# Performance work log

Hardware: AMD Instinct MI355X
Metric: run time of the kernel (lower is better)

Reference implementation:

```python
import jax, jax.numpy as jnp
import numpy as np

HEIGHT = 108
WIDTH = 108
LEN_CLASSES = 7
EPS = 1e-5


def layout_bbox(pred, H, W):
    # pred: [B, O, 4 + LEN_CLASSES]
    bbox = pred[..., :4]
    cls_prob = pred[..., 4:]  # [B,O,7]
    x_c = bbox[..., 0] * W   # [B,O]
    y_c = bbox[..., 1] * H
    w = bbox[..., 2] * W
    h = bbox[..., 3] * H
    x1 = (x_c - 0.5 * w)[:, :, None, None]  # [B,O,1,1]
    x2 = (x_c + 0.5 * w)[:, :, None, None]
    y1 = (y_c - 0.5 * h)[:, :, None, None]
    y2 = (y_c + 0.5 * h)[:, :, None, None]
    xt = jnp.arange(W, dtype=pred.dtype)[None, None, None, :]  # [1,1,1,W]
    yt = jnp.arange(H, dtype=pred.dtype)[None, None, :, None]  # [1,1,H,1]
    x1d = xt - x1  # [B,O,1,W]
    x2d = x2 - xt
    y1d = yt - y1  # [B,O,H,1]
    y2d = y2 - yt
    # min(relu(d), 1) == clip(d, 0, 1)
    yband = jnp.clip(y1d, 0.0, 1.0) * jnp.clip(y2d, 0.0, 1.0)  # [B,O,H,1]
    xband = jnp.clip(x1d, 0.0, 1.0) * jnp.clip(x2d, 0.0, 1.0)  # [B,O,1,W]
    x1_line = jax.nn.relu(1.0 - jnp.abs(x1d)) * yband  # [B,O,H,W]
    x2_line = jax.nn.relu(1.0 - jnp.abs(x2d)) * yband
    y1_line = jax.nn.relu(1.0 - jnp.abs(y1d)) * xband
    y2_line = jax.nn.relu(1.0 - jnp.abs(y2d)) * xband
    xy_max = jnp.maximum(jnp.maximum(x1_line, x2_line), jnp.maximum(y1_line, y2_line))  # [B,O,H,W]
    spatial = xy_max[..., None] * cls_prob[:, :, None, None, :]  # [B,O,H,W,7]
    return jnp.max(spatial, axis=1)  # [B,H,W,7]


def bn(x, g, b, axes):
    m = jnp.mean(x, axis=axes, keepdims=True)
    v = jnp.var(x, axis=axes, keepdims=True)
    shape = [1] * x.ndim
    shape[1 if x.ndim == 4 else -1] = -1
    return (x - m) * jax.lax.rsqrt(v + EPS) * g.reshape(shape) + b.reshape(shape)


def conv2d(x, w, b, stride):
    y = jax.lax.conv_general_dilated(x, w, (stride, stride), 'VALID',
                                     dimension_numbers=('NCHW', 'OIHW', 'NCHW'))
    return y + b[None, :, None, None]


def setup_inputs() -> dict:
    key = jax.random.key(0)
    ks = jax.random.split(key, 16)
    B, O = 64, 16
    d = {}
    d['image'] = jax.random.uniform(ks[0], (B, O, 4 + LEN_CLASSES), dtype=jnp.float32)
    d['conv1_w'] = jax.random.normal(ks[1], (32, LEN_CLASSES, 5, 5), jnp.float32) * 0.05
    d['conv1_b'] = jnp.zeros((32,), jnp.float32)
    d['bn1_g'] = jnp.ones((32,), jnp.float32)
    d['bn1_b'] = jnp.zeros((32,), jnp.float32)
    d['conv2_w'] = jax.random.normal(ks[2], (64, 32, 5, 5), jnp.float32) * 0.03
    d['conv2_b'] = jnp.zeros((64,), jnp.float32)
    d['bn2_g'] = jnp.ones((64,), jnp.float32)
    d['bn2_b'] = jnp.zeros((64,), jnp.float32)
    d['fc1_w'] = jax.random.normal(ks[3], (512, 36864), jnp.float32) * 0.005
    d['fc1_b'] = jnp.zeros((512,), jnp.float32)
    d['bn3_g'] = jnp.ones((512,), jnp.float32)
    d['bn3_b'] = jnp.zeros((512,), jnp.float32)
    d['fc2_w'] = jax.random.normal(ks[4], (1, 512), jnp.float32) * 0.04
    d['fc2_b'] = jnp.zeros((1,), jnp.float32)
    return d


def reference(image, conv1_w, conv1_b, bn1_g, bn1_b, conv2_w, conv2_b, bn2_g, bn2_b,
              fc1_w, fc1_b, bn3_g, bn3_b, fc2_w, fc2_b):
    # layout_bbox(image, WIDTH, HEIGHT): output_height=WIDTH, output_width=HEIGHT (both 108)
    layout = layout_bbox(image, WIDTH, HEIGHT)           # [B,108,108,7]
    x = jnp.transpose(layout, (0, 3, 1, 2))              # [B,7,108,108]
    x = conv2d(x, conv1_w, conv1_b, 2)                   # [B,32,52,52]
    x = bn(x, bn1_g, bn1_b, (0, 2, 3))
    x = jax.nn.leaky_relu(x, 0.2)
    x = conv2d(x, conv2_w, conv2_b, 2)                   # [B,64,24,24]
    x = bn(x, bn2_g, bn2_b, (0, 2, 3))
    x = jax.nn.leaky_relu(x, 0.2)
    x = x.reshape(x.shape[0], -1)                        # [B,36864]
    x = x @ fc1_w.T + fc1_b                              # [B,512]
    x = bn(x, bn3_g, bn3_b, (0,))
    x = jax.nn.leaky_relu(x, 0.2)
    x = x @ fc2_w.T + fc2_b                              # [B,1]
    return jax.nn.sigmoid(x)
```

## Files before the change

kernel.cpp:

```cpp
#include <hip/hip_runtime.h>
#include <hip/hip_bf16.h>


typedef unsigned short u16;
typedef __attribute__((ext_vector_type(8))) short bf8_t;
typedef __attribute__((ext_vector_type(4))) float f4_t;
#define MFMA16(a, b, c) __builtin_amdgcn_mfma_f32_16x16x32_bf16(a, b, c, 0, 0, 0)

#define LEAKY(v) (fmaxf((v), 0.2f * (v)))
#define CLIP01(v) fminf(fmaxf((v), 0.0f), 1.0f)

__device__ inline unsigned f2bf(float f) {
  unsigned u = __float_as_uint(f);
  return (u + 0x7FFFu + ((u >> 16) & 1u)) >> 16;
}
__device__ inline float bf2f(unsigned u) {
  return __uint_as_float(u << 16);
}

constexpr int HW = 108;
constexpr int NOBJ = 16;
constexpr int NCLS = 7;

__global__ __launch_bounds__(128) void layout_kernel(
    const float* __restrict__ image, u16* __restrict__ lay8) {
  int h = blockIdx.x, b = blockIdx.y;
  __shared__ float sIm[NOBJ * 11];
  int tid = threadIdx.x;
  for (int i = tid; i < NOBJ * 11; i += 128) sIm[i] = image[b * NOBJ * 11 + i];
  __syncthreads();
  int w = tid;
  if (w >= HW) return;
  float best[NCLS];
#pragma unroll
  for (int c = 0; c < NCLS; ++c) best[c] = 0.0f;
  float fw = (float)w, fh = (float)h;
  for (int o = 0; o < NOBJ; ++o) {
    const float* p = &sIm[o * 11];
    float xc = p[0] * 108.0f, yc = p[1] * 108.0f;
    float wd = p[2] * 108.0f, hd = p[3] * 108.0f;
    float x1 = xc - 0.5f * wd, x2 = xc + 0.5f * wd;
    float y1 = yc - 0.5f * hd, y2 = yc + 0.5f * hd;
    float x1d = fw - x1, x2d = x2 - fw;
    float y1d = fh - y1, y2d = y2 - fh;
    float yband = CLIP01(y1d) * CLIP01(y2d);
    float xband = CLIP01(x1d) * CLIP01(x2d);
    float x1l = fmaxf(1.0f - fabsf(x1d), 0.0f) * yband;
    float x2l = fmaxf(1.0f - fabsf(x2d), 0.0f) * yband;
    float y1l = fmaxf(1.0f - fabsf(y1d), 0.0f) * xband;
    float y2l = fmaxf(1.0f - fabsf(y2d), 0.0f) * xband;
    float xy = fmaxf(fmaxf(x1l, x2l), fmaxf(y1l, y2l));
#pragma unroll
    for (int c = 0; c < NCLS; ++c) best[c] = fmaxf(best[c], xy * p[4 + c]);
  }
  unsigned p0 = f2bf(best[0]) | (f2bf(best[1]) << 16);
  unsigned p1 = f2bf(best[2]) | (f2bf(best[3]) << 16);
  unsigned p2 = f2bf(best[4]) | (f2bf(best[5]) << 16);
  unsigned p3 = f2bf(best[6]);
  uint4 st = {p0, p1, p2, p3};
  ((uint4*)lay8)[b * 11664 + h * 108 + w] = st;
}

__global__ __launch_bounds__(256) void wprep_kernel(
    const float* __restrict__ w1, const float* __restrict__ w2,
    u16* __restrict__ wB1, u16* __restrict__ wB2) {
  int i = blockIdx.x * 256 + threadIdx.x;
  if (i < 7168) {
    int co = i / 224, k = i % 224;
    int chunk = k >> 5, kk = k & 31, tl = kk >> 3, ci = kk & 7;
    int tap = chunk * 4 + tl;
    unsigned v = 0;
    if (tap < 25 && ci < 7) v = f2bf(w1[co * 175 + ci * 25 + tap]);
    wB1[i] = (u16)v;
  } else {
    int j = i - 7168;
    int tap = j / 2048, r = j % 2048, co = r >> 5, ci = r & 31;
    wB2[j] = (u16)f2bf(w2[co * 800 + ci * 25 + tap]);
  }
}

__global__ __launch_bounds__(128) void conv1_mfma(
    const u16* __restrict__ lay8, const u16* __restrict__ wB1,
    u16* __restrict__ x1r, float* __restrict__ bn1sum,
    float* __restrict__ bn1sq) {
  int strip = blockIdx.x, b = blockIdx.y;
  int tid = threadIdx.x;
  int lane = tid & 63, wv = tid >> 6;
  int f = lane & 15, q = lane >> 4;
  int co = wv * 16 + f;
  int pbase[13];
#pragma unroll
  for (int t = 0; t < 13; ++t) {
    int P = strip * 208 + t * 16 + f;
    int oh = P / 52, ow = P - oh * 52;
    pbase[t] = (oh * 2 * 108 + ow * 2) * 8;
  }
  const u16* lb = lay8 + (size_t)b * 93312;
  f4_t acc[13];
#pragma unroll
  for (int t = 0; t < 13; ++t) acc[t] = {0.f, 0.f, 0.f, 0.f};
#pragma unroll
  for (int chunk = 0; chunk < 7; ++chunk) {
    int tap = chunk * 4 + q;
    tap = tap > 24 ? 24 : tap;
    int kh = tap / 5, kw = tap - kh * 5;
    int toff = (kh * 108 + kw) * 8;
    bf8_t bf = *(const bf8_t*)&wB1[co * 224 + chunk * 32 + q * 8];
    bf8_t af[13];
#pragma unroll
    for (int t = 0; t < 13; ++t) af[t] = *(const bf8_t*)&lb[pbase[t] + toff];
#pragma unroll
    for (int t = 0; t < 13; ++t) acc[t] = MFMA16(af[t], bf, acc[t]);
  }
  u16* ob = x1r + (size_t)b * 86528;
  float s = 0.f, sq = 0.f;
#pragma unroll
  for (int t = 0; t < 13; ++t) {
#pragma unroll
    for (int r = 0; r < 4; ++r) {
      float v = acc[t][r];
      s += v;
      sq += v * v;
      int P = strip * 208 + t * 16 + q * 4 + r;
      ob[P * 32 + co] = (u16)f2bf(v);
    }
  }
  s += __shfl_xor(s, 16);
  s += __shfl_xor(s, 32);
  sq += __shfl_xor(sq, 16);
  sq += __shfl_xor(sq, 32);
  if (lane < 16) {
    atomicAdd(&bn1sum[co], s);
    atomicAdd(&bn1sq[co], sq);
  }
}

__global__ void bn_finalize_kernel(
    const float* __restrict__ sum, const float* __restrict__ sumsq,
    const float* __restrict__ g, const float* __restrict__ bb, float invN,
    int C, float* __restrict__ scale, float* __restrict__ shift) {
  int c = threadIdx.x;
  if (c < C) {
    float mean = sum[c] * invN;
    float var = sumsq[c] * invN - mean * mean;
    float sc = g[c] * rsqrtf(var + 1e-5f);
    scale[c] = sc;
    shift[c] = bb[c] - mean * sc;
  }
}

__global__ __launch_bounds__(256) void bnapply1_kernel(
    const u16* __restrict__ x1r, const float* __restrict__ sc,
    const float* __restrict__ sh, u16* __restrict__ x1b) {
  int idx = blockIdx.x * 256 + threadIdx.x;
  int base = idx * 8, c0 = base & 31;
  uint4 in = *(const uint4*)&x1r[base];
  unsigned w[4] = {in.x, in.y, in.z, in.w};
  unsigned out[4];
#pragma unroll
  for (int j = 0; j < 4; ++j) {
    float a = bf2f(w[j] & 0xffffu);
    float bq = bf2f(w[j] >> 16);
    a = LEAKY(fmaf(a, sc[c0 + 2 * j], sh[c0 + 2 * j]));
    bq = LEAKY(fmaf(bq, sc[c0 + 2 * j + 1], sh[c0 + 2 * j + 1]));
    out[j] = f2bf(a) | (f2bf(bq) << 16);
  }
  uint4 st = {out[0], out[1], out[2], out[3]};
  *(uint4*)&x1b[base] = st;
}

__global__ __launch_bounds__(256) void conv2_mfma(
    const u16* __restrict__ x1b, const u16* __restrict__ wB2,
    float* __restrict__ x2c, float* __restrict__ bn2sum,
    float* __restrict__ bn2sq) {
  int strip = blockIdx.x, b = blockIdx.y;
  int tid = threadIdx.x;
  int lane = tid & 63, wv = tid >> 6;
  int f = lane & 15, q = lane >> 4;
  int mbase = (wv >> 1) * 3, nbase = (wv & 1) * 2;
  int pbase[3];
#pragma unroll
  for (int t = 0; t < 3; ++t) {
    int P = strip * 96 + (mbase + t) * 16 + f;
    int oh = P / 24, ow = P - oh * 24;
    pbase[t] = (oh * 2 * 52 + ow * 2) * 32 + q * 8;
  }
  const u16* xb = x1b + (size_t)b * 86528;
  f4_t acc[3][2];
#pragma unroll
  for (int t = 0; t < 3; ++t)
#pragma unroll
    for (int n = 0; n < 2; ++n) acc[t][n] = {0.f, 0.f, 0.f, 0.f};
#pragma unroll
  for (int tap = 0; tap < 25; ++tap) {
    int kh = tap / 5, kw = tap - kh * 5;
    int toff = (kh * 52 + kw) * 32;
    bf8_t bfr[2];
#pragma unroll
    for (int n = 0; n < 2; ++n)
      bfr[n] =
          *(const bf8_t*)&wB2[tap * 2048 + ((nbase + n) * 16 + f) * 32 + q * 8];
    bf8_t afr[3];
#pragma unroll
    for (int t = 0; t < 3; ++t) afr[t] = *(const bf8_t*)&xb[pbase[t] + toff];
#pragma unroll
    for (int t = 0; t < 3; ++t)
#pragma unroll
      for (int n = 0; n < 2; ++n) acc[t][n] = MFMA16(afr[t], bfr[n], acc[t][n]);
  }
  float* ob = x2c + (size_t)b * 576 * 64;
  float s[2] = {0.f, 0.f}, sq[2] = {0.f, 0.f};
#pragma unroll
  for (int t = 0; t < 3; ++t)
#pragma unroll
    for (int n = 0; n < 2; ++n)
#pragma unroll
      for (int r = 0; r < 4; ++r) {
        float v = acc[t][n][r];
        s[n] += v;
        sq[n] += v * v;
        int P = strip * 96 + (mbase + t) * 16 + q * 4 + r;
        ob[P * 64 + (nbase + n) * 16 + f] = v;
      }
#pragma unroll
  for (int n = 0; n < 2; ++n) {
    s[n] += __shfl_xor(s[n], 16);
    s[n] += __shfl_xor(s[n], 32);
    sq[n] += __shfl_xor(sq[n], 16);
    sq[n] += __shfl_xor(sq[n], 32);
  }
  if (lane < 16) {
#pragma unroll
    for (int n = 0; n < 2; ++n) {
      int c = (nbase + n) * 16 + f;
      atomicAdd(&bn2sum[c], s[n]);
      atomicAdd(&bn2sq[c], sq[n]);
    }
  }
}

__global__ __launch_bounds__(256) void bnapply2t_kernel(
    const float* __restrict__ x2c, const float* __restrict__ sc2,
    const float* __restrict__ sh2, u16* __restrict__ xB) {
  int hw0 = blockIdx.x * 64, b = blockIdx.y;
  __shared__ float tile[64 * 65];
  int t = threadIdx.x;
  int c = t & 63, hl4 = t >> 6;
  float s = sc2[c], h = sh2[c];
#pragma unroll
  for (int it = 0; it < 16; ++it) {
    int hl = it * 4 + hl4;
    float v = x2c[((size_t)b * 576 + hw0 + hl) * 64 + c];
    tile[hl * 65 + c] = LEAKY(fmaf(v, s, h));
  }
  __syncthreads();
  int hw = t & 63, cl4 = t >> 6;
#pragma unroll
  for (int it = 0; it < 16; ++it) {
    int cc = it * 4 + cl4;
    xB[(size_t)b * 36864 + cc * 576 + hw0 + hw] = (u16)f2bf(tile[hw * 65 + cc]);
  }
}

__global__ __launch_bounds__(256) void fc1_mfma(
    const u16* __restrict__ xB, const float* __restrict__ wgt,
    float* __restrict__ part) {
  int ks = blockIdx.x, nb = blockIdx.y;
  int tid = threadIdx.x;
  int lane = tid & 63, wv = tid >> 6;
  int f = lane & 15, q = lane >> 4;
  int n0 = nb * 64 + wv * 16;
  int kbase = ks * 512;
  __shared__ u16 sA[64 * 520];
#pragma unroll
  for (int i = 0; i < 16; ++i) {
    int c = i * 256 + tid;
    int row = c >> 6, col = c & 63;
    *(uint4*)&sA[row * 520 + col * 8] =
        *(const uint4*)&xB[(size_t)row * 36864 + kbase + col * 8];
  }
  __syncthreads();
  f4_t acc[4];
#pragma unroll
  for (int m = 0; m < 4; ++m) acc[m] = {0.f, 0.f, 0.f, 0.f};
  const float* wrow = wgt + (size_t)(n0 + f) * 36864 + kbase + q * 8;
#pragma unroll 4
  for (int kt = 0; kt < 16; ++kt) {
    const float* wp = wrow + kt * 32;
    float4 wa = *(const float4*)wp;
    float4 wb = *(const float4*)(wp + 4);
    union { bf8_t v; u16 u[8]; } bu;
    bu.u[0] = (u16)f2bf(wa.x); bu.u[1] = (u16)f2bf(wa.y);
    bu.u[2] = (u16)f2bf(wa.z); bu.u[3] = (u16)f2bf(wa.w);
    bu.u[4] = (u16)f2bf(wb.x); bu.u[5] = (u16)f2bf(wb.y);
    bu.u[6] = (u16)f2bf(wb.z); bu.u[7] = (u16)f2bf(wb.w);
    bf8_t afr[4];
#pragma unroll
    for (int m = 0; m < 4; ++m)
      afr[m] = *(const bf8_t*)&sA[(m * 16 + f) * 520 + kt * 32 + q * 8];
#pragma unroll
    for (int m = 0; m < 4; ++m) acc[m] = MFMA16(afr[m], bu.v, acc[m]);
  }
  float* pp = part + (size_t)ks * 32768;
#pragma unroll
  for (int m = 0; m < 4; ++m)
#pragma unroll
    for (int r = 0; r < 4; ++r)
      pp[(m * 16 + q * 4 + r) * 512 + n0 + f] = acc[m][r];
}

__global__ __launch_bounds__(256) void fc1_reduce_kernel(
    const float* __restrict__ part, float* __restrict__ out) {
  int i = blockIdx.x * 256 + threadIdx.x;
  float s = 0.f;
#pragma unroll 8
  for (int ks = 0; ks < 72; ++ks) s += part[(size_t)ks * 32768 + i];
  out[i] = s;
}

__global__ __launch_bounds__(64) void bn3_kernel(
    const float* __restrict__ fc1o, const float* __restrict__ g,
    const float* __restrict__ bb, float* __restrict__ scale,
    float* __restrict__ shift) {
  int f = blockIdx.x * 64 + threadIdx.x;
  float s = 0.f, q = 0.f;
  for (int m = 0; m < 64; ++m) {
    float v = fc1o[m * 512 + f];
    s += v;
    q += v * v;
  }
  float mean = s * (1.f / 64.f);
  float var = q * (1.f / 64.f) - mean * mean;
  float sc = g[f] * rsqrtf(var + 1e-5f);
  scale[f] = sc;
  shift[f] = bb[f] - mean * sc;
}

__global__ __launch_bounds__(64) void fc2_kernel(
    const float* __restrict__ fc1o, const float* __restrict__ sc,
    const float* __restrict__ sh, const float* __restrict__ w2,
    const float* __restrict__ b2, float* __restrict__ out) {
  int m = blockIdx.x;
  int f = threadIdx.x;
  float acc = 0.f;
#pragma unroll
  for (int j = 0; j < 8; ++j) {
    int ff = f + j * 64;
    float v = fc1o[m * 512 + ff] * sc[ff] + sh[ff];
    v = LEAKY(v);
    acc += v * w2[ff];
  }
  for (int off = 32; off; off >>= 1) acc += __shfl_down(acc, off, 64);
  if (f == 0) out[m] = 1.f / (1.f + expf(-(acc + b2[0])));
}

extern "C" void kernel_launch(void* const* d_in, const int* in_sizes, int n_in,
                              void* d_out, int out_size, void* d_ws,
                              size_t ws_size, hipStream_t stream) {
  const float* image = (const float*)d_in[0];
  const float* c1w = (const float*)d_in[1];
  const float* bn1g = (const float*)d_in[3];
  const float* bn1b = (const float*)d_in[4];
  const float* c2w = (const float*)d_in[5];
  const float* bn2g = (const float*)d_in[7];
  const float* bn2b = (const float*)d_in[8];
  const float* f1w = (const float*)d_in[9];
  const float* bn3g = (const float*)d_in[11];
  const float* bn3b = (const float*)d_in[12];
  const float* f2w = (const float*)d_in[13];
  const float* f2b = (const float*)d_in[14];
  float* ws = (float*)d_ws;

  u16* lay8 = (u16*)ws;
  u16* x1b = (u16*)ws;
  u16* x1r = (u16*)(ws + 2985984);
  float* x2c = ws + 2985984;
  float* fc1part = ws + 2985984;
  u16* xB = (u16*)(ws + 5345280);
  float* fc1o = ws + 6524928;
  float* st = ws + 6557696;
  float* bn1sum = st, *bn1sq = st + 32, *bn2sum = st + 64, *bn2sq = st + 128;
  float* coef = ws + 6557888;
  float* sc1 = coef, *sh1 = coef + 32;
  float* sc2 = coef + 64, *sh2 = coef + 128;
  float* sc3 = coef + 192, *sh3 = coef + 704;
  u16* wB1 = (u16*)(ws + 6559104);
  u16* wB2 = (u16*)(ws + 6562688);

  hipMemsetAsync(st, 0, 192 * sizeof(float), stream);

  wprep_kernel<<<228, 256, 0, stream>>>(c1w, c2w, wB1, wB2);
  layout_kernel<<<dim3(108, 64), 128, 0, stream>>>(image, lay8);
  conv1_mfma<<<dim3(13, 64), 128, 0, stream>>>(lay8, wB1, x1r, bn1sum, bn1sq);
  bn_finalize_kernel<<<1, 64, 0, stream>>>(bn1sum, bn1sq, bn1g, bn1b,
                                           1.f / 173056.f, 32, sc1, sh1);
  bnapply1_kernel<<<2704, 256, 0, stream>>>(x1r, sc1, sh1, x1b);
  conv2_mfma<<<dim3(6, 64), 256, 0, stream>>>(x1b, wB2, x2c, bn2sum, bn2sq);
  bn_finalize_kernel<<<1, 64, 0, stream>>>(bn2sum, bn2sq, bn2g, bn2b,
                                           1.f / 36864.f, 64, sc2, sh2);
  bnapply2t_kernel<<<dim3(9, 64), 256, 0, stream>>>(x2c, sc2, sh2, xB);
  fc1_mfma<<<dim3(72, 8), 256, 0, stream>>>(xB, f1w, fc1part);
  fc1_reduce_kernel<<<128, 256, 0, stream>>>(fc1part, fc1o);
  bn3_kernel<<<8, 64, 0, stream>>>(fc1o, bn3g, bn3b, sc3, sh3);
  fc2_kernel<<<64, 64, 0, stream>>>(fc1o, sc3, sh3, f2w, f2b, (float*)d_out);
}
```

Baseline: 256.4 us.

## Fuse BN finalize/apply into consumer kernels and cut launch count

Removes the standalone BN finalize, bn1-apply, fc1-reduce and bn3 kernels, plus the memset. BN1 scale/shift is now computed per block inside conv2 and applied to the raw conv1 activations on load. BN2 finalize moves into bnapply2t, and fc1 reduce, BN3 and leaky are merged into one finish kernel. Conv2 is re-tiled to 16-pixel tiles over 36x64 blocks of 128 threads, and the stats zeroing is folded into wprep. The aim is fewer launches and no extra pass over the conv1 activations, at the cost of redundant BN math per tap and per block, and a reduction in only 8 blocks.

```diff
diff --git a/kernel.cpp b/kernel.cpp
--- a/kernel.cpp
+++ b/kernel.cpp
@@ -14,9 +14,7 @@
   unsigned u = __float_as_uint(f);
   return (u + 0x7FFFu + ((u >> 16) & 1u)) >> 16;
 }
-__device__ inline float bf2f(unsigned u) {
-  return __uint_as_float(u << 16);
-}
+__device__ inline float bf2f(unsigned u) { return __uint_as_float(u << 16); }
 
 constexpr int HW = 108;
 constexpr int NOBJ = 16;
@@ -63,8 +61,9 @@
 
 __global__ __launch_bounds__(256) void wprep_kernel(
     const float* __restrict__ w1, const float* __restrict__ w2,
-    u16* __restrict__ wB1, u16* __restrict__ wB2) {
+    u16* __restrict__ wB1, u16* __restrict__ wB2, float* __restrict__ st) {
   int i = blockIdx.x * 256 + threadIdx.x;
+  if (i < 192) st[i] = 0.f;
   if (i < 7168) {
     int co = i / 224, k = i % 224;
     int chunk = k >> 5, kk = k & 31, tl = kk >> 3, ci = kk & 7;
@@ -72,7 +71,7 @@
     unsigned v = 0;
     if (tap < 25 && ci < 7) v = f2bf(w1[co * 175 + ci * 25 + tap]);
     wB1[i] = (u16)v;
-  } else {
+  } else if (i < 58368) {
     int j = i - 7168;
     int tap = j / 2048, r = j % 2048, co = r >> 5, ci = r & 31;
     wB2[j] = (u16)f2bf(w2[co * 800 + ci * 25 + tap]);
@@ -135,118 +134,91 @@
   }
 }
 
-__global__ void bn_finalize_kernel(
-    const float* __restrict__ sum, const float* __restrict__ sumsq,
-    const float* __restrict__ g, const float* __restrict__ bb, float invN,
-    int C, float* __restrict__ scale, float* __restrict__ shift) {
-  int c = threadIdx.x;
-  if (c < C) {
-    float mean = sum[c] * invN;
-    float var = sumsq[c] * invN - mean * mean;
-    float sc = g[c] * rsqrtf(var + 1e-5f);
-    scale[c] = sc;
-    shift[c] = bb[c] - mean * sc;
-  }
-}
-
-__global__ __launch_bounds__(256) void bnapply1_kernel(
-    const u16* __restrict__ x1r, const float* __restrict__ sc,
-    const float* __restrict__ sh, u16* __restrict__ x1b) {
-  int idx = blockIdx.x * 256 + threadIdx.x;
-  int base = idx * 8, c0 = base & 31;
-  uint4 in = *(const uint4*)&x1r[base];
-  unsigned w[4] = {in.x, in.y, in.z, in.w};
-  unsigned out[4];
-#pragma unroll
-  for (int j = 0; j < 4; ++j) {
-    float a = bf2f(w[j] & 0xffffu);
-    float bq = bf2f(w[j] >> 16);
-    a = LEAKY(fmaf(a, sc[c0 + 2 * j], sh[c0 + 2 * j]));
-    bq = LEAKY(fmaf(bq, sc[c0 + 2 * j + 1], sh[c0 + 2 * j + 1]));
-    out[j] = f2bf(a) | (f2bf(bq) << 16);
-  }
-  uint4 st = {out[0], out[1], out[2], out[3]};
-  *(uint4*)&x1b[base] = st;
-}
-
-__global__ __launch_bounds__(256) void conv2_mfma(
-    const u16* __restrict__ x1b, const u16* __restrict__ wB2,
+__global__ __launch_bounds__(128) void conv2_mfma(
+    const u16* __restrict__ x1r, const u16* __restrict__ wB2,
+    const float* __restrict__ bn1sum, const float* __restrict__ bn1sq,
+    const float* __restrict__ g1, const float* __restrict__ b1,
     float* __restrict__ x2c, float* __restrict__ bn2sum,
     float* __restrict__ bn2sq) {
-  int strip = blockIdx.x, b = blockIdx.y;
+  int mt = blockIdx.x, b = blockIdx.y;
   int tid = threadIdx.x;
   int lane = tid & 63, wv = tid >> 6;
   int f = lane & 15, q = lane >> 4;
-  int mbase = (wv >> 1) * 3, nbase = (wv & 1) * 2;
-  int pbase[3];
-#pragma unroll
-  for (int t = 0; t < 3; ++t) {
-    int P = strip * 96 + (mbase + t) * 16 + f;
-    int oh = P / 24, ow = P - oh * 24;
-    pbase[t] = (oh * 2 * 52 + ow * 2) * 32 + q * 8;
-  }
-  const u16* xb = x1b + (size_t)b * 86528;
-  f4_t acc[3][2];
-#pragma unroll
-  for (int t = 0; t < 3; ++t)
-#pragma unroll
-    for (int n = 0; n < 2; ++n) acc[t][n] = {0.f, 0.f, 0.f, 0.f};
+  float sc[8], sh[8];
+#pragma unroll
+  for (int j = 0; j < 8; ++j) {
+    int c = q * 8 + j;
+    float mean = bn1sum[c] * (1.f / 173056.f);
+    float var = bn1sq[c] * (1.f / 173056.f) - mean * mean;
+    float s = g1[c] * rsqrtf(var + 1e-5f);
+    sc[j] = s;
+    sh[j] = b1[c] - mean * s;
+  }
+  int P = mt * 16 + f;
+  int oh = P / 24, ow = P - oh * 24;
+  const u16* ap =
+      x1r + (size_t)b * 86528 + (oh * 2 * 52 + ow * 2) * 32 + q * 8;
+  f4_t acc[2];
+  acc[0] = {0.f, 0.f, 0.f, 0.f};
+  acc[1] = {0.f, 0.f, 0.f, 0.f};
 #pragma unroll
   for (int tap = 0; tap < 25; ++tap) {
     int kh = tap / 5, kw = tap - kh * 5;
-    int toff = (kh * 52 + kw) * 32;
-    bf8_t bfr[2];
-#pragma unroll
-    for (int n = 0; n < 2; ++n)
-      bfr[n] =
-          *(const bf8_t*)&wB2[tap * 2048 + ((nbase + n) * 16 + f) * 32 + q * 8];
-    bf8_t afr[3];
-#pragma unroll
-    for (int t = 0; t < 3; ++t) afr[t] = *(const bf8_t*)&xb[pbase[t] + toff];
-#pragma unroll
-    for (int t = 0; t < 3; ++t)
-#pragma unroll
-      for (int n = 0; n < 2; ++n) acc[t][n] = MFMA16(afr[t], bfr[n], acc[t][n]);
+    bf8_t araw = *(const bf8_t*)(ap + (kh * 52 + kw) * 32);
+    union { bf8_t v; u16 u[8]; } au;
+#pragma unroll
+    for (int j = 0; j < 8; ++j) {
+      float v = bf2f((unsigned)(u16)araw[j]);
+      v = LEAKY(fmaf(v, sc[j], sh[j]));
+      au.u[j] = (u16)f2bf(v);
+    }
+    bf8_t bf0 = *(const bf8_t*)&wB2[tap * 2048 + (wv * 32 + f) * 32 + q * 8];
+    bf8_t bf1 =
+        *(const bf8_t*)&wB2[tap * 2048 + (wv * 32 + 16 + f) * 32 + q * 8];
+    acc[0] = MFMA16(au.v, bf0, acc[0]);
+    acc[1] = MFMA16(au.v, bf1, acc[1]);
   }
   float* ob = x2c + (size_t)b * 576 * 64;
-  float s[2] = {0.f, 0.f}, sq[2] = {0.f, 0.f};
-#pragma unroll
-  for (int t = 0; t < 3; ++t)
-#pragma unroll
-    for (int n = 0; n < 2; ++n)
-#pragma unroll
-      for (int r = 0; r < 4; ++r) {
-        float v = acc[t][n][r];
-        s[n] += v;
-        sq[n] += v * v;
-        int P = strip * 96 + (mbase + t) * 16 + q * 4 + r;
-        ob[P * 64 + (nbase + n) * 16 + f] = v;
-      }
+  float s2[2] = {0.f, 0.f}, q2[2] = {0.f, 0.f};
+#pragma unroll
+  for (int n = 0; n < 2; ++n)
+#pragma unroll
+    for (int r = 0; r < 4; ++r) {
+      float v = acc[n][r];
+      s2[n] += v;
+      q2[n] += v * v;
+      int Pr = mt * 16 + q * 4 + r;
+      ob[Pr * 64 + wv * 32 + n * 16 + f] = v;
+    }
 #pragma unroll
   for (int n = 0; n < 2; ++n) {
-    s[n] += __shfl_xor(s[n], 16);
-    s[n] += __shfl_xor(s[n], 32);
-    sq[n] += __shfl_xor(sq[n], 16);
-    sq[n] += __shfl_xor(sq[n], 32);
+    s2[n] += __shfl_xor(s2[n], 16);
+    s2[n] += __shfl_xor(s2[n], 32);
+    q2[n] += __shfl_xor(q2[n], 16);
+    q2[n] += __shfl_xor(q2[n], 32);
   }
   if (lane < 16) {
 #pragma unroll
     for (int n = 0; n < 2; ++n) {
-      int c = (nbase + n) * 16 + f;
-      atomicAdd(&bn2sum[c], s[n]);
-      atomicAdd(&bn2sq[c], sq[n]);
+      int c = wv * 32 + n * 16 + f;
+      atomicAdd(&bn2sum[c], s2[n]);
+      atomicAdd(&bn2sq[c], q2[n]);
     }
   }
 }
 
 __global__ __launch_bounds__(256) void bnapply2t_kernel(
-    const float* __restrict__ x2c, const float* __restrict__ sc2,
-    const float* __restrict__ sh2, u16* __restrict__ xB) {
+    const float* __restrict__ x2c, const float* __restrict__ bn2sum,
+    const float* __restrict__ bn2sq, const float* __restrict__ g2,
+    const float* __restrict__ b2, u16* __restrict__ xB) {
   int hw0 = blockIdx.x * 64, b = blockIdx.y;
   __shared__ float tile[64 * 65];
   int t = threadIdx.x;
   int c = t & 63, hl4 = t >> 6;
-  float s = sc2[c], h = sh2[c];
+  float mean = bn2sum[c] * (1.f / 36864.f);
+  float var = bn2sq[c] * (1.f / 36864.f) - mean * mean;
+  float s = g2[c] * rsqrtf(var + 1e-5f);
+  float h = b2[c] - mean * s;
 #pragma unroll
   for (int it = 0; it < 16; ++it) {
     int hl = it * 4 + hl4;
@@ -309,49 +281,61 @@
       pp[(m * 16 + q * 4 + r) * 512 + n0 + f] = acc[m][r];
 }
 
-__global__ __launch_bounds__(256) void fc1_reduce_kernel(
-    const float* __restrict__ part, float* __restrict__ out) {
-  int i = blockIdx.x * 256 + threadIdx.x;
-  float s = 0.f;
+__global__ __launch_bounds__(256) void fc1_finish_kernel(
+    const float* __restrict__ part, const float* __restrict__ g,
+    const float* __restrict__ bb, float* __restrict__ act) {
+  int bx = blockIdx.x;
+  int t = threadIdx.x;
+  int fl = t & 63, mg = t >> 6;
+  int f = bx * 64 + fl;
+  __shared__ float sAct[64 * 64];
+  __shared__ float sSum[4 * 64], sSq[4 * 64];
+  __shared__ float sC[64], sH[64];
+  float psum = 0.f, psq = 0.f;
+  for (int mi = 0; mi < 16; ++mi) {
+    int m = mg * 16 + mi;
+    float s = 0.f;
 #pragma unroll 8
-  for (int ks = 0; ks < 72; ++ks) s += part[(size_t)ks * 32768 + i];
-  out[i] = s;
-}
-
-__global__ __launch_bounds__(64) void bn3_kernel(
-    const float* __restrict__ fc1o, const float* __restrict__ g,
-    const float* __restrict__ bb, float* __restrict__ scale,
-    float* __restrict__ shift) {
-  int f = blockIdx.x * 64 + threadIdx.x;
-  float s = 0.f, q = 0.f;
-  for (int m = 0; m < 64; ++m) {
-    float v = fc1o[m * 512 + f];
-    s += v;
-    q += v * v;
-  }
-  float mean = s * (1.f / 64.f);
-  float var = q * (1.f / 64.f) - mean * mean;
-  float sc = g[f] * rsqrtf(var + 1e-5f);
-  scale[f] = sc;
-  shift[f] = bb[f] - mean * sc;
+    for (int ks = 0; ks < 72; ++ks)
+      s += part[(size_t)ks * 32768 + m * 512 + f];
+    sAct[m * 64 + fl] = s;
+    psum += s;
+    psq += s * s;
+  }
+  sSum[mg * 64 + fl] = psum;
+  sSq[mg * 64 + fl] = psq;
+  __syncthreads();
+  if (t < 64) {
+    float s = sSum[t] + sSum[64 + t] + sSum[128 + t] + sSum[192 + t];
+    float qq = sSq[t] + sSq[64 + t] + sSq[128 + t] + sSq[192 + t];
+    float mean = s * (1.f / 64.f);
+    float var = qq * (1.f / 64.f) - mean * mean;
+    float scv = g[bx * 64 + t] * rsqrtf(var + 1e-5f);
+    sC[t] = scv;
+    sH[t] = bb[bx * 64 + t] - mean * scv;
+  }
+  __syncthreads();
+  float scv = sC[fl], shv = sH[fl];
+  for (int mi = 0; mi < 16; ++mi) {
+    int m = mg * 16 + mi;
+    float v = fmaf(sAct[m * 64 + fl], scv, shv);
+    act[m * 512 + f] = LEAKY(v);
+  }
 }
 
 __global__ __launch_bounds__(64) void fc2_kernel(
-    const float* __restrict__ fc1o, const float* __restrict__ sc,
-    const float* __restrict__ sh, const float* __restrict__ w2,
+    const float* __restrict__ act, const float* __restrict__ w2,
     const float* __restrict__ b2, float* __restrict__ out) {
   int m = blockIdx.x;
-  int f = threadIdx.x;
-  float acc = 0.f;
+  int fl = threadIdx.x;
+  float a = 0.f;
 #pragma unroll
   for (int j = 0; j < 8; ++j) {
-    int ff = f + j * 64;
-    float v = fc1o[m * 512 + ff] * sc[ff] + sh[ff];
-    v = LEAKY(v);
-    acc += v * w2[ff];
-  }
-  for (int off = 32; off; off >>= 1) acc += __shfl_down(acc, off, 64);
-  if (f == 0) out[m] = 1.f / (1.f + expf(-(acc + b2[0])));
+    int ff = fl + j * 64;
+    a += act[m * 512 + ff] * w2[ff];
+  }
+  for (int off = 32; off; off >>= 1) a += __shfl_down(a, off, 64);
+  if (fl == 0) out[m] = 1.f / (1.f + expf(-(a + b2[0])));
 }
 
 extern "C" void kernel_launch(void* const* d_in, const int* in_sizes, int n_in,
@@ -372,35 +356,24 @@
   float* ws = (float*)d_ws;
 
   u16* lay8 = (u16*)ws;
-  u16* x1b = (u16*)ws;
+  float* fc1part = ws;
   u16* x1r = (u16*)(ws + 2985984);
-  float* x2c = ws + 2985984;
-  float* fc1part = ws + 2985984;
-  u16* xB = (u16*)(ws + 5345280);
-  float* fc1o = ws + 6524928;
-  float* st = ws + 6557696;
+  float* x2c = ws + 5754880;
+  u16* xB = (u16*)(ws + 8114176);
+  float* act = ws + 9293824;
+  float* st = ws + 9326592;
   float* bn1sum = st, *bn1sq = st + 32, *bn2sum = st + 64, *bn2sq = st + 128;
-  float* coef = ws + 6557888;
-  float* sc1 = coef, *sh1 = coef + 32;
-  float* sc2 = coef + 64, *sh2 = coef + 128;
-  float* sc3 = coef + 192, *sh3 = coef + 704;
-  u16* wB1 = (u16*)(ws + 6559104);
-  u16* wB2 = (u16*)(ws + 6562688);
-
-  hipMemsetAsync(st, 0, 192 * sizeof(float), stream);
-
-  wprep_kernel<<<228, 256, 0, stream>>>(c1w, c2w, wB1, wB2);
+  u16* wB1 = (u16*)(ws + 9326784);
+  u16* wB2 = (u16*)(ws + 9330368);
+
+  wprep_kernel<<<228, 256, 0, stream>>>(c1w, c2w, wB1, wB2, st);
   layout_kernel<<<dim3(108, 64), 128, 0, stream>>>(image, lay8);
   conv1_mfma<<<dim3(13, 64), 128, 0, stream>>>(lay8, wB1, x1r, bn1sum, bn1sq);
-  bn_finalize_kernel<<<1, 64, 0, stream>>>(bn1sum, bn1sq, bn1g, bn1b,
-                                           1.f / 173056.f, 32, sc1, sh1);
-  bnapply1_kernel<<<2704, 256, 0, stream>>>(x1r, sc1, sh1, x1b);
-  conv2_mfma<<<dim3(6, 64), 256, 0, stream>>>(x1b, wB2, x2c, bn2sum, bn2sq);
-  bn_finalize_kernel<<<1, 64, 0, stream>>>(bn2sum, bn2sq, bn2g, bn2b,
-                                           1.f / 36864.f, 64, sc2, sh2);
-  bnapply2t_kernel<<<dim3(9, 64), 256, 0, stream>>>(x2c, sc2, sh2, xB);
+  conv2_mfma<<<dim3(36, 64), 128, 0, stream>>>(x1r, wB2, bn1sum, bn1sq, bn1g,
+                                               bn1b, x2c, bn2sum, bn2sq);
+  bnapply2t_kernel<<<dim3(9, 64), 256, 0, stream>>>(x2c, bn2sum, bn2sq, bn2g,
+                                                    bn2b, xB);
   fc1_mfma<<<dim3(72, 8), 256, 0, stream>>>(xB, f1w, fc1part);
-  fc1_reduce_kernel<<<128, 256, 0, stream>>>(fc1part, fc1o);
-  bn3_kernel<<<8, 64, 0, stream>>>(fc1o, bn3g, bn3b, sc3, sh3);
-  fc2_kernel<<<64, 64, 0, stream>>>(fc1o, sc3, sh3, f2w, f2b, (float*)d_out);
-}
+  fc1_finish_kernel<<<8, 256, 0, stream>>>(fc1part, bn3g, bn3b, act);
+  fc2_kernel<<<64, 64, 0, stream>>>(act, f2w, f2b, (float*)d_out);
+}
```

Result: slower. 342.0 us (+33.4%).
